# Optimization experiments

Measured on AMD Instinct MI355X. Metric: run time of the kernel, lower is better.

Reference implementation:

```python
import jax, jax.numpy as jnp
import numpy as np
from jax import lax

RF, NLF, MESH, FUSION = 64, 16, 16, 64


def _conv3x3(x, w, b):
    # stride 1, pad 1, ksize 3 == SAME
    y = lax.conv_general_dilated(x, w, (1, 1), 'SAME',
                                 dimension_numbers=('NCHW', 'OIHW', 'NCHW'))
    return y + b[None, :, None, None]


def _bn(x, g, b, m, v, eps=1e-5):
    scale = g / jnp.sqrt(v + eps)
    return (x - m[None, :, None, None]) * scale[None, :, None, None] + b[None, :, None, None]


def _rct_block(x, w1, b1, g, be, m, v, w2, b2):
    # extra_conv=True: Conv -> BN -> SiLU -> Conv (all stride 1)
    h = jax.nn.silu(_bn(_conv3x3(x, w1, b1), g, be, m, v))
    return _conv3x3(h, w2, b2)


def setup_inputs():
    key = jax.random.key(0)
    ks = jax.random.split(key, 8)
    B, H, W = 4, 512, 512
    return {
        'feature': jax.random.normal(ks[0], (B, RF, H, W), jnp.float32),
        'p_low': jax.random.normal(ks[1], (B, FUSION, MESH + 1, MESH + 1), jnp.float32),
        'r_w1': jax.random.normal(ks[2], (FUSION, FUSION, 3, 3), jnp.float32) * 0.05,
        'r_b1': jnp.zeros((FUSION,), jnp.float32),
        'r_gamma': jnp.ones((FUSION,), jnp.float32),
        'r_beta': jnp.zeros((FUSION,), jnp.float32),
        'r_mean': jnp.zeros((FUSION,), jnp.float32),
        'r_var': jnp.ones((FUSION,), jnp.float32),
        'r_w2': jax.random.normal(ks[3], (RF * NLF, FUSION, 3, 3), jnp.float32) * 0.05,
        'r_b2': jnp.zeros((RF * NLF,), jnp.float32),
        't_w1': jax.random.normal(ks[4], (FUSION, FUSION, 3, 3), jnp.float32) * 0.05,
        't_b1': jnp.zeros((FUSION,), jnp.float32),
        't_gamma': jnp.ones((FUSION,), jnp.float32),
        't_beta': jnp.zeros((FUSION,), jnp.float32),
        't_mean': jnp.zeros((FUSION,), jnp.float32),
        't_var': jnp.ones((FUSION,), jnp.float32),
        't_w2': jax.random.normal(ks[5], (3 * NLF, FUSION, 3, 3), jnp.float32) * 0.05,
        't_b2': jnp.zeros((3 * NLF,), jnp.float32),
    }


def reference(feature, p_low, r_w1, r_b1, r_gamma, r_beta, r_mean, r_var, r_w2, r_b2,
              t_w1, t_b1, t_gamma, t_beta, t_mean, t_var, t_w2, t_b2):
    B, C, H, W = feature.shape
    M = MESH
    mh, mw = H // M, W // M  # H,W divisible by mesh_size -> pad_tensor is identity
    P = mh * mw

    r_l = _rct_block(p_low, r_w1, r_b1, r_gamma, r_beta, r_mean, r_var, r_w2, r_b2)  # [B, RF*NLF, M+1, M+1]
    t_l = _rct_block(p_low, t_w1, t_b1, t_gamma, t_beta, t_mean, t_var, t_w2, t_b2)  # [B, 3*NLF, M+1, M+1]

    # channel dim factors as (feat, nlf); corners concat along nlf axis in order
    # (i,j), (i,j+1), (i+1,j), (i+1,j+1) -> K = 4*NLF keys per tile
    rc = r_l.reshape(B, RF, NLF, M + 1, M + 1)
    rk = jnp.concatenate([rc[..., :M, :M], rc[..., :M, 1:],
                          rc[..., 1:, :M], rc[..., 1:, 1:]], axis=2)  # [B,RF,4NLF,M,M]
    tc = t_l.reshape(B, 3, NLF, M + 1, M + 1)
    tk = jnp.concatenate([tc[..., :M, :M], tc[..., :M, 1:],
                          tc[..., 1:, :M], tc[..., 1:, 1:]], axis=2)  # [B,3,4NLF,M,M]

    # split feature into tiles: [B, M, M, P, RF] (row-major pixel order within tile)
    f = feature.reshape(B, RF, M, mh, M, mw).transpose(0, 2, 4, 3, 5, 1).reshape(B, M, M, P, RF)

    scale = 1.0 / jnp.sqrt(jnp.float32(RF))
    att = jnp.einsum('bxypr,brkxy->bxypk', f, rk) * scale  # [B,M,M,P,4NLF]
    att = jax.nn.softmax(att, axis=-1)
    out = jnp.einsum('bxypk,bckxy->bxycp', att, tk)  # [B,M,M,3,P]

    Y = out.reshape(B, M, M, 3, mh, mw).transpose(0, 3, 1, 4, 2, 5).reshape(B, 3, H, W)
    return Y
```

## Files before the change

kernel.cpp:

```cpp
#include <hip/hip_runtime.h>

typedef unsigned short u16;
typedef __bf16 bf16x8 __attribute__((ext_vector_type(8)));
typedef unsigned short us8 __attribute__((ext_vector_type(8)));
typedef float f32x4 __attribute__((ext_vector_type(4)));
typedef float f32x2 __attribute__((ext_vector_type(2)));
typedef unsigned int u32x4 __attribute__((ext_vector_type(4)));

union U8u { us8 s; u16 u[8]; };

__device__ __forceinline__ u16 f2bf(float f){
  unsigned u = __builtin_bit_cast(unsigned, f);
  u += 0x7fffu + ((u >> 16) & 1u);
  return (u16)(u >> 16);
}
__device__ __forceinline__ bf16x8 asbf(us8 x){ return __builtin_bit_cast(bf16x8, x); }

#define MFMA16(a,b,c) __builtin_amdgcn_mfma_f32_16x16x32_bf16((a),(b),(c),0,0,0)

__device__ __forceinline__ void stage_zero2(u16* sS, int tid){
  uint* z = (uint*)sS;
  for (int i = tid; i < 12996; i += 256) z[i] = 0u;
}

__device__ __forceinline__ void stage_src_f32T(const float* __restrict__ src,
                                               u16* sS, int tid){
  for (int i4 = tid; i4 < 4624; i4 += 256){
    int e = i4 * 4;
    f32x4 dv = *(const f32x4*)(src + e);
    #pragma unroll
    for (int t = 0; t < 4; t++){
      int ee = e + t;
      int ci = ee / 289; int rr = ee - ci*289;
      int oy = rr / 17;  int ox = rr - oy*17;
      sS[((oy+1)*19 + ox+1)*72 + ci] = f2bf(dv[t]);
    }
  }
}

__device__ __forceinline__ void stage_src_pm(const u16* __restrict__ src,
                                             u16* sS, int tid){
  for (int i8 = tid; i8 < 2312; i8 += 256){
    int pix = i8 >> 3, c0 = (i8 & 7) << 3;
    us8 v = *(const us8*)(src + ((size_t)pix << 6) + c0);
    int oy = pix / 17, ox = pix - oy*17;
    *(us8*)(sS + ((oy+1)*19 + ox+1)*72 + c0) = v;
  }
}

__device__ __forceinline__ void stage_w_f32(const float* __restrict__ w, int m0,
                                            u16* sW, int tid){
  for (int i4 = tid; i4 < 2304; i4 += 256){
    int e = i4 * 4;
    int co = e / 576; int r0 = e - co*576;
    f32x4 wv = *(const f32x4*)(w + (size_t)(m0+co)*576 + r0);
    #pragma unroll
    for (int t = 0; t < 4; t++){
      int r = r0 + t; int cin = r / 9; int tap = r - cin*9;
      sW[co*584 + tap*64 + cin] = f2bf(wv[t]);
    }
  }
}

__device__ __forceinline__ f32x4 conv_tile2(const u16* sS, const u16* sW,
                                            int nt, int l15, int q)
{
  int p = nt*16 + l15; int pc = p > 288 ? 288 : p;
  int oy = pc / 17, ox = pc - oy*17;
  f32x4 acc = {0.f, 0.f, 0.f, 0.f};
  #pragma unroll
  for (int ks = 0; ks < 18; ks++){
    const int tap = ks >> 1;
    const int dy = tap / 3, dx = tap - dy*3;
    int pix2 = (oy+dy)*19 + (ox+dx);
    us8 bv = *(const us8*)(sS + pix2*72 + (ks & 1)*32 + q*8);
    us8 av = *(const us8*)(sW + l15*584 + ks*32 + q*8);
    acc = MFMA16(asbf(av), asbf(bv), acc);
  }
  return acc;
}

__global__ __launch_bounds__(256) void conv1_k(
    const float* __restrict__ p_low,
    const float* __restrict__ wR, const float* __restrict__ b1R,
    const float* __restrict__ gR, const float* __restrict__ beR,
    const float* __restrict__ mR, const float* __restrict__ vR,
    const float* __restrict__ wT, const float* __restrict__ b1T,
    const float* __restrict__ gT, const float* __restrict__ beT,
    const float* __restrict__ mT, const float* __restrict__ vT,
    u16* __restrict__ hR, u16* __restrict__ hT)
{
  __shared__ __attribute__((aligned(16))) u16 sS[25992];
  __shared__ __attribute__((aligned(16))) u16 sW[9344];
  int tid = threadIdx.x;
  int bx = blockIdx.x;
  int job = bx >> 4;
  int b = (bx >> 2) & 3;
  int m0 = (bx & 3) << 4;
  const float* w  = job ? wT  : wR;
  const float* b1 = job ? b1T : b1R;
  const float* g  = job ? gT  : gR;
  const float* be = job ? beT : beR;
  const float* mn = job ? mT  : mR;
  const float* vr = job ? vT  : vR;
  u16* out = job ? hT : hR;
  const float* src = p_low + (size_t)b * 18496;

  stage_zero2(sS, tid);
  __syncthreads();
  stage_src_f32T(src, sS, tid);
  stage_w_f32(w, m0, sW, tid);
  __syncthreads();

  int lane = tid & 63, wave = tid >> 6;
  int l15 = lane & 15, q = lane >> 4;
  float scl[4], sft[4];
  #pragma unroll
  for (int e = 0; e < 4; e++){
    int co = m0 + q*4 + e;
    float s = g[co] / sqrtf(vr[co] + 1e-5f);
    scl[e] = s;
    sft[e] = (b1[co] - mn[co]) * s + be[co];
  }
  for (int nt = wave; nt < 19; nt += 4){
    f32x4 acc = conv_tile2(sS, sW, nt, l15, q);
    int p = nt*16 + l15;
    if (p < 289){
      float si[4];
      #pragma unroll
      for (int e = 0; e < 4; e++){
        float y = acc[e]*scl[e] + sft[e];
        si[e] = y / (1.f + __expf(-y));
      }
      uint2 pk;
      pk.x = (uint)f2bf(si[0]) | ((uint)f2bf(si[1]) << 16);
      pk.y = (uint)f2bf(si[2]) | ((uint)f2bf(si[3]) << 16);
      *(uint2*)(out + ((size_t)b*289 + p)*64 + m0 + q*4) = pk;
    }
  }
}

__global__ __launch_bounds__(256) void conv2_k(
    const u16* __restrict__ hR, const u16* __restrict__ hT,
    const float* __restrict__ w2R, const float* __restrict__ b2R,
    const float* __restrict__ w2T, const float* __restrict__ b2T,
    u16* __restrict__ rlq, float* __restrict__ tlq)
{
  __shared__ __attribute__((aligned(16))) u16 sS[25992];
  __shared__ __attribute__((aligned(16))) u16 sW[9344];
  int tid = threadIdx.x;
  int bx = blockIdx.x;
  const float *w, *bias; const u16* src;
  int b, m0, isR;
  if (bx < 256){
    isR = 1; b = bx >> 6; m0 = (bx & 63) << 4;
    src = hR + (size_t)b*18496; w = w2R; bias = b2R;
  } else {
    isR = 0; int i = bx - 256; b = i / 3; m0 = (i - b*3) << 4;
    src = hT + (size_t)b*18496; w = w2T; bias = b2T;
  }

  stage_zero2(sS, tid);
  __syncthreads();
  stage_src_pm(src, sS, tid);
  stage_w_f32(w, m0, sW, tid);
  __syncthreads();

  int lane = tid & 63, wave = tid >> 6;
  int l15 = lane & 15, q = lane >> 4;
  float bs[4];
  #pragma unroll
  for (int e = 0; e < 4; e++) bs[e] = bias[m0 + q*4 + e];
  const float PSC = 0.18033688f;
  for (int nt = wave; nt < 19; nt += 4){
    f32x4 acc = conv_tile2(sS, sW, nt, l15, q);
    int p = nt*16 + l15;
    if (p < 289){
      if (isR){
        uint2 pk;
        pk.x = (uint)f2bf((acc[0]+bs[0])*PSC)
             | ((uint)f2bf((acc[1]+bs[1])*PSC) << 16);
        pk.y = (uint)f2bf((acc[2]+bs[2])*PSC)
             | ((uint)f2bf((acc[3]+bs[3])*PSC) << 16);
        *(uint2*)(rlq + ((size_t)b*289 + p)*1024 + m0 + q*4) = pk;
      } else {
        f32x4 ov = {acc[0]+bs[0], acc[1]+bs[1], acc[2]+bs[2], acc[3]+bs[3]};
        *(f32x4*)(tlq + ((size_t)b*289 + p)*48 + m0 + q*4) = ov;
      }
    }
  }
}

__global__ __launch_bounds__(256) void attn_k(
    const uint* __restrict__ feat,
    const u16* __restrict__ rlq, const float* __restrict__ tlq,
    float* __restrict__ out)
{
  __shared__ __attribute__((aligned(16))) u16 rkT[4608];
  __shared__ __attribute__((aligned(16))) float tkF[256];
  int tid = threadIdx.x;
  int ty = blockIdx.x, tx = blockIdx.y, b = blockIdx.z;
  int lane = tid & 63, wave = tid >> 6;
  int l15 = lane & 15, q = lane >> 4;

  {
    int corner = wave;
    int pix = (tx + (corner >> 1))*17 + ty + (corner & 1);
    const u16* sp = rlq + ((size_t)b*289 + pix)*1024 + lane*16;
    U8u v0, v1; v0.s = *(const us8*)sp; v1.s = *(const us8*)(sp + 8);
    #pragma unroll
    for (int nl = 0; nl < 8; nl++){
      rkT[(corner*16 + nl)*72 + lane]     = v0.u[nl];
      rkT[(corner*16 + 8 + nl)*72 + lane] = v1.u[nl];
    }
  }
  if (tid < 192){
    int corner = tid / 48; int idx = tid - corner*48;
    int pix = (tx + (corner >> 1))*17 + ty + (corner & 1);
    int c = idx >> 4, nl = idx & 15;
    tkF[c*64 + corner*16 + nl] = tlq[((size_t)b*289 + pix)*48 + idx];
  }
  __syncthreads();

  bf16x8 frk[4][2];
  #pragma unroll
  for (int nt = 0; nt < 4; nt++)
    #pragma unroll
    for (int ks = 0; ks < 2; ks++)
      frk[nt][ks] = __builtin_bit_cast(bf16x8,
          *(const us8*)(rkT + (nt*16 + l15)*72 + ks*32 + q*8));

  f32x4 tkc[3][4];
  #pragma unroll
  for (int c = 0; c < 3; c++)
    #pragma unroll
    for (int nt = 0; nt < 4; nt++)
      tkc[c][nt] = *(const f32x4*)(tkF + c*64 + nt*16 + q*4);

  const uint HW = 512u*512u;
  const uint* fpb = feat + (size_t)b*64*HW;
  uint offbase = (uint)(q*8)*HW + (uint)(tx*32 + wave*8)*512u
               + (uint)(ty*32 + l15);

  uint r0[8], r1[8];
  #pragma unroll
  for (int j = 0; j < 8; j++){
    r0[j] = fpb[offbase + (uint)j*HW];
    r1[j] = fpb[offbase + (uint)(j+32)*HW];
  }

  #pragma unroll
  for (int cnk = 0; cnk < 16; cnk++){
    u32x4 p0v, p1v;
    #pragma unroll
    for (int j2 = 0; j2 < 4; j2++){
      p0v[j2] = __builtin_amdgcn_perm(r0[2*j2+1], r0[2*j2], 0x07060302u);
      p1v[j2] = __builtin_amdgcn_perm(r1[2*j2+1], r1[2*j2], 0x07060302u);
    }
    bf16x8 A0 = __builtin_bit_cast(bf16x8, p0v);
    bf16x8 A1 = __builtin_bit_cast(bf16x8, p1v);

    if (cnk < 15){
      int nc = cnk + 1;
      uint noff = offbase + (uint)((nc >> 1)*512 + ((nc & 1) << 4));
      #pragma unroll
      for (int j = 0; j < 8; j++){
        r0[j] = fpb[noff + (uint)j*HW];
        r1[j] = fpb[noff + (uint)(j+32)*HW];
      }
    }

    f32x4 acc[4];
    __builtin_amdgcn_s_setprio(1);
    #pragma unroll
    for (int nt = 0; nt < 4; nt++){
      f32x4 zz = {0.f, 0.f, 0.f, 0.f};
      zz = MFMA16(frk[nt][0], A0, zz);
      zz = MFMA16(frk[nt][1], A1, zz);
      acc[nt] = zz;
    }
    __builtin_amdgcn_s_setprio(0);

    f32x2 den2 = {0.f,0.f}, o0v = {0.f,0.f}, o1v = {0.f,0.f}, o2v = {0.f,0.f};
    #pragma unroll
    for (int nt = 0; nt < 4; nt++){
      f32x2 pa, pb;
      pa[0] = __builtin_amdgcn_exp2f(acc[nt][0]);
      pa[1] = __builtin_amdgcn_exp2f(acc[nt][1]);
      pb[0] = __builtin_amdgcn_exp2f(acc[nt][2]);
      pb[1] = __builtin_amdgcn_exp2f(acc[nt][3]);
      den2 += pa; den2 += pb;
      f32x2 t0a = {tkc[0][nt][0], tkc[0][nt][1]};
      f32x2 t0b = {tkc[0][nt][2], tkc[0][nt][3]};
      f32x2 t1a = {tkc[1][nt][0], tkc[1][nt][1]};
      f32x2 t1b = {tkc[1][nt][2], tkc[1][nt][3]};
      f32x2 t2a = {tkc[2][nt][0], tkc[2][nt][1]};
      f32x2 t2b = {tkc[2][nt][2], tkc[2][nt][3]};
      o0v = __builtin_elementwise_fma(pa, t0a, o0v);
      o0v = __builtin_elementwise_fma(pb, t0b, o0v);
      o1v = __builtin_elementwise_fma(pa, t1a, o1v);
      o1v = __builtin_elementwise_fma(pb, t1b, o1v);
      o2v = __builtin_elementwise_fma(pa, t2a, o2v);
      o2v = __builtin_elementwise_fma(pb, t2b, o2v);
    }
    float den = den2[0] + den2[1];
    float o0 = o0v[0] + o0v[1];
    float o1 = o1v[0] + o1v[1];
    float o2 = o2v[0] + o2v[1];
    o0  += __shfl_xor(o0, 16, 64);
    o1  += __shfl_xor(o1, 16, 64);
    o2  += __shfl_xor(o2, 16, 64);
    den += __shfl_xor(den, 16, 64);
    o0  += __shfl_xor(o0, 32, 64);
    o1  += __shfl_xor(o1, 32, 64);
    o2  += __shfl_xor(o2, 32, 64);
    den += __shfl_xor(den, 32, 64);
    float rin = __builtin_amdgcn_rcpf(den);
    float val = (q == 0) ? o0 : ((q == 1) ? o1 : o2);
    int hh = tx*32 + wave*8 + (cnk >> 1);
    int j0 = (cnk & 1) << 4;
    if (q < 3)
      out[((size_t)(b*3 + q)*512 + hh)*512 + (ty*32 + j0 + l15)] = val * rin;
  }
}

extern "C" void kernel_launch(void* const* d_in, const int* in_sizes, int n_in,
                              void* d_out, int out_size, void* d_ws, size_t ws_size,
                              hipStream_t stream)
{
  (void)in_sizes; (void)n_in; (void)out_size; (void)ws_size;
  const uint*  feature = (const uint*)d_in[0];
  const float* p_low = (const float*)d_in[1];
  const float* r_w1 = (const float*)d_in[2];
  const float* r_b1 = (const float*)d_in[3];
  const float* r_g  = (const float*)d_in[4];
  const float* r_be = (const float*)d_in[5];
  const float* r_m  = (const float*)d_in[6];
  const float* r_v  = (const float*)d_in[7];
  const float* r_w2 = (const float*)d_in[8];
  const float* r_b2 = (const float*)d_in[9];
  const float* t_w1 = (const float*)d_in[10];
  const float* t_b1 = (const float*)d_in[11];
  const float* t_g  = (const float*)d_in[12];
  const float* t_be = (const float*)d_in[13];
  const float* t_m  = (const float*)d_in[14];
  const float* t_v  = (const float*)d_in[15];
  const float* t_w2 = (const float*)d_in[16];
  const float* t_b2 = (const float*)d_in[17];

  char* ws = (char*)d_ws;
  u16* hR = (u16*)ws;
  u16* hT = hR + (size_t)4*289*64;
  u16* rlq = (u16*)(ws + 295936);
  float* tlq = (float*)(ws + 295936 + 2367488);
  float* outp = (float*)d_out;

  hipLaunchKernelGGL(conv1_k, dim3(32), dim3(256), 0, stream,
      p_low, r_w1, r_b1, r_g, r_be, r_m, r_v,
      t_w1, t_b1, t_g, t_be, t_m, t_v, hR, hT);
  hipLaunchKernelGGL(conv2_k, dim3(268), dim3(256), 0, stream,
      hR, hT, r_w2, r_b2, t_w2, t_b2, rlq, tlq);
  hipLaunchKernelGGL(attn_k, dim3(16, 16, 4), dim3(256), 0, stream,
      feature, rlq, tlq, outp);
}
```

Measured before the change: 445.1 us.

## Split conv1 across pixel tiles and trim attention register pressure

conv1 now runs on 128 blocks instead of 32, with each block handling one quarter of the output pixel tiles. This spreads a tiny kernel over more CUs, at the cost of each block re-staging the full source and weights into shared memory. In the attention kernel, the tk values are reloaded from LDS on every chunk instead of being held in 48 registers, which is meant to free VGPRs. Feature loads now use per-channel base pointers with an incrementing offset, to simplify address arithmetic.

```diff
diff --git a/kernel.cpp b/kernel.cpp
--- a/kernel.cpp
+++ b/kernel.cpp
@@ -94,9 +94,11 @@
   __shared__ __attribute__((aligned(16))) u16 sW[9344];
   int tid = threadIdx.x;
   int bx = blockIdx.x;
-  int job = bx >> 4;
-  int b = (bx >> 2) & 3;
-  int m0 = (bx & 3) << 4;
+  int job = bx >> 6;
+  int b = (bx >> 4) & 3;
+  int m0 = ((bx >> 2) & 3) << 4;
+  int px = bx & 3;
+  int nt0 = px * 5, ntEnd = nt0 + 5 > 19 ? 19 : nt0 + 5;
   const float* w  = job ? wT  : wR;
   const float* b1 = job ? b1T : b1R;
   const float* g  = job ? gT  : gR;
@@ -122,7 +124,7 @@
     scl[e] = s;
     sft[e] = (b1[co] - mn[co]) * s + be[co];
   }
-  for (int nt = wave; nt < 19; nt += 4){
+  for (int nt = nt0 + wave; nt < ntEnd; nt += 4){
     f32x4 acc = conv_tile2(sS, sW, nt, l15, q);
     int p = nt*16 + l15;
     if (p < 289){
@@ -230,23 +232,23 @@
       frk[nt][ks] = __builtin_bit_cast(bf16x8,
           *(const us8*)(rkT + (nt*16 + l15)*72 + ks*32 + q*8));
 
-  f32x4 tkc[3][4];
-  #pragma unroll
-  for (int c = 0; c < 3; c++)
-    #pragma unroll
-    for (int nt = 0; nt < 4; nt++)
-      tkc[c][nt] = *(const f32x4*)(tkF + c*64 + nt*16 + q*4);
+  const float* __restrict__ tkq = tkF + q*4;
 
   const uint HW = 512u*512u;
   const uint* fpb = feat + (size_t)b*64*HW;
-  uint offbase = (uint)(q*8)*HW + (uint)(tx*32 + wave*8)*512u
-               + (uint)(ty*32 + l15);
+  const uint* fb0[8]; const uint* fb1[8];
+  #pragma unroll
+  for (int j = 0; j < 8; j++){
+    fb0[j] = fpb + (size_t)j*HW;
+    fb1[j] = fpb + (size_t)(j+32)*HW;
+  }
+  uint offv = (uint)(q*8)*HW + (uint)(tx*32 + wave*8)*512u + (uint)(ty*32 + l15);
 
   uint r0[8], r1[8];
   #pragma unroll
   for (int j = 0; j < 8; j++){
-    r0[j] = fpb[offbase + (uint)j*HW];
-    r1[j] = fpb[offbase + (uint)(j+32)*HW];
+    r0[j] = fb0[j][offv];
+    r1[j] = fb1[j][offv];
   }
 
   #pragma unroll
@@ -261,12 +263,11 @@
     bf16x8 A1 = __builtin_bit_cast(bf16x8, p1v);
 
     if (cnk < 15){
-      int nc = cnk + 1;
-      uint noff = offbase + (uint)((nc >> 1)*512 + ((nc & 1) << 4));
+      offv += (cnk & 1) ? 496u : 16u;
       #pragma unroll
       for (int j = 0; j < 8; j++){
-        r0[j] = fpb[noff + (uint)j*HW];
-        r1[j] = fpb[noff + (uint)(j+32)*HW];
+        r0[j] = fb0[j][offv];
+        r1[j] = fb1[j][offv];
       }
     }
 
@@ -284,18 +285,18 @@
     f32x2 den2 = {0.f,0.f}, o0v = {0.f,0.f}, o1v = {0.f,0.f}, o2v = {0.f,0.f};
     #pragma unroll
     for (int nt = 0; nt < 4; nt++){
+      f32x4 t0 = *(const f32x4*)(tkq + 0*64 + nt*16);
+      f32x4 t1 = *(const f32x4*)(tkq + 1*64 + nt*16);
+      f32x4 t2 = *(const f32x4*)(tkq + 2*64 + nt*16);
       f32x2 pa, pb;
       pa[0] = __builtin_amdgcn_exp2f(acc[nt][0]);
       pa[1] = __builtin_amdgcn_exp2f(acc[nt][1]);
       pb[0] = __builtin_amdgcn_exp2f(acc[nt][2]);
       pb[1] = __builtin_amdgcn_exp2f(acc[nt][3]);
       den2 += pa; den2 += pb;
-      f32x2 t0a = {tkc[0][nt][0], tkc[0][nt][1]};
-      f32x2 t0b = {tkc[0][nt][2], tkc[0][nt][3]};
-      f32x2 t1a = {tkc[1][nt][0], tkc[1][nt][1]};
-      f32x2 t1b = {tkc[1][nt][2], tkc[1][nt][3]};
-      f32x2 t2a = {tkc[2][nt][0], tkc[2][nt][1]};
-      f32x2 t2b = {tkc[2][nt][2], tkc[2][nt][3]};
+      f32x2 t0a = {t0[0], t0[1]}, t0b = {t0[2], t0[3]};
+      f32x2 t1a = {t1[0], t1[1]}, t1b = {t1[2], t1[3]};
+      f32x2 t2a = {t2[0], t2[1]}, t2b = {t2[2], t2[3]};
       o0v = __builtin_elementwise_fma(pa, t0a, o0v);
       o0v = __builtin_elementwise_fma(pb, t0b, o0v);
       o1v = __builtin_elementwise_fma(pa, t1a, o1v);
@@ -355,7 +356,7 @@
   float* tlq = (float*)(ws + 295936 + 2367488);
   float* outp = (float*)d_out;
 
-  hipLaunchKernelGGL(conv1_k, dim3(32), dim3(256), 0, stream,
+  hipLaunchKernelGGL(conv1_k, dim3(128), dim3(256), 0, stream,
       p_low, r_w1, r_b1, r_g, r_be, r_m, r_v,
       t_w1, t_b1, t_g, t_be, t_m, t_v, hR, hT);
   hipLaunchKernelGGL(conv2_k, dim3(268), dim3(256), 0, stream,
```

Measured after the change: 446.4 us. Within noise of the previous version (+0.3%).
